# Kernel optimization log

Measured on AMD Instinct MI355X. Metric: run time of the kernel, lower is better.

The kernel has to match this reference:

```python
import jax, jax.numpy as jnp
import numpy as np

B, T, D, H, L = 2, 2048, 2048, 16, 64
HD = D // H  # 128
EPS = 1e-5


def setup_inputs() -> dict:
    key = jax.random.key(0)
    ks = jax.random.split(key, 16)
    s = 0.02
    inp = {
        'x': jax.random.normal(ks[0], (B, T, D), jnp.float32),
        'mask': jnp.tril(jnp.ones((T, T), dtype=bool)),
        'ln_w': jnp.ones((D,), jnp.float32),
        'ln_b': jnp.zeros((D,), jnp.float32),
        'wq': jax.random.normal(ks[1], (D, D), jnp.float32) * s,
        'bq': jnp.zeros((D,), jnp.float32),
        'wk': jax.random.normal(ks[2], (D, D), jnp.float32) * s,
        'bk': jnp.zeros((D,), jnp.float32),
        'wv': jax.random.normal(ks[3], (D, D), jnp.float32) * s,
        'bv': jnp.zeros((D,), jnp.float32),
        'wo': jax.random.normal(ks[4], (D, D), jnp.float32) * s,
        'bo': jnp.zeros((D,), jnp.float32),
        'wcq': jax.random.normal(ks[5], (HD, L), jnp.float32) * s,
        'bcq': jnp.zeros((L,), jnp.float32),
        'wck': jax.random.normal(ks[6], (HD, L), jnp.float32) * s,
        'bck': jnp.zeros((L,), jnp.float32),
        'wcv': jax.random.normal(ks[7], (HD, L), jnp.float32) * s,
        'bcv': jnp.zeros((L,), jnp.float32),
        'wd': jax.random.normal(ks[8], (L, HD), jnp.float32) * s,
        'bd': jnp.zeros((HD,), jnp.float32),
    }
    # standard RoPE frequency table: theta_i = 10000^{-2i/HD}
    inv_freq = 1.0 / (10000.0 ** (jnp.arange(0, HD, 2, dtype=jnp.float32) / HD))
    ang = jnp.arange(T, dtype=jnp.float32)[:, None] * inv_freq[None, :]  # [T, HD/2]
    inp['freqs_cos'] = jnp.cos(ang)
    inp['freqs_sin'] = jnp.sin(ang)
    return inp


def _rope(x, cos, sin):
    # x: [B,T,H,HD]; cos/sin: [T, HD/2]; interleaved (even=real, odd=imag)
    xr, xi = x[..., 0::2], x[..., 1::2]
    c = cos[None, :, None, :]
    sn = sin[None, :, None, :]
    out_r = xr * c - xi * sn
    out_i = xr * sn + xi * c
    return jnp.stack([out_r, out_i], axis=-1).reshape(x.shape)


def reference(x, mask, freqs_cos, freqs_sin, ln_w, ln_b, wq, bq, wk, bk, wv, bv,
              wo, bo, wcq, bcq, wck, bck, wcv, bcv, wd, bd):
    # LayerNorm
    mu = jnp.mean(x, axis=-1, keepdims=True)
    var = jnp.mean(jnp.square(x - mu), axis=-1, keepdims=True)
    xn = (x - mu) / jnp.sqrt(var + EPS) * ln_w + ln_b

    q = (xn @ wq + bq).reshape(B, T, H, HD)
    k = (xn @ wk + bk).reshape(B, T, H, HD)
    v = (xn @ wv + bv).reshape(B, T, H, HD)

    q, k = _rope(q, freqs_cos, freqs_sin), _rope(k, freqs_cos, freqs_sin)

    # compress each head to the latent dim
    q_lat = q @ wcq + bcq  # [B,T,H,L]
    k_lat = k @ wck + bck
    v_lat = v @ wcv + bcv

    scale = 1.0 / np.sqrt(L).astype(np.float32)
    scores = jnp.einsum('bqhl,bkhl->bhqk', q_lat, k_lat) * scale  # [B,H,T,T]
    additive = jnp.where(mask, 0.0, -1e9).astype(scores.dtype)  # bool mask -> additive
    scores = scores + additive[None, None, :, :]
    attn = jax.nn.softmax(scores, axis=-1)

    out = jnp.einsum('bhqk,bkhl->bqhl', attn, v_lat)  # [B,T,H,L]
    out = (out @ wd + bd).reshape(B, T, D)  # decompress to head_dim, merge heads
    return out @ wo + bo
```

## Files before the change

### kernel.cpp

```cpp
#include <hip/hip_runtime.h>
#include <hip/hip_bf16.h>
#include <stdint.h>

#define BB 2
#define TB 2048
#define DB 2048
#define HB 16
#define HDB 128
#define LB 64
#define MB 4096

typedef __hip_bfloat16 bf16;
typedef __attribute__((ext_vector_type(8))) short bf16x8;
typedef __attribute__((ext_vector_type(4))) float f32x4;

#define MFMA_16x16x32 __builtin_amdgcn_mfma_f32_16x16x32_bf16

typedef __attribute__((address_space(3))) void lds_t;
typedef const __attribute__((address_space(1))) void gvm_t;

static __device__ __forceinline__ float bf2f(bf16 h) { return __bfloat162float(h); }
static __device__ __forceinline__ bf16 f2bf(float f) { return __float2bfloat16(f); }
union BV8 { bf16x8 v; bf16 e[8]; };
union BV4 { ushort4 v; bf16 e[4]; };

#define SWZC(r) (((r) ^ ((r) >> 3)) & 7)

__device__ void do_ln(const float* __restrict__ x, const float* __restrict__ g,
                      const float* __restrict__ be, bf16* __restrict__ xn,
                      int row, int tid, char* sm) {
  float* red = (float*)sm;
  const float4* xr = (const float4*)(x + (size_t)row * DB);
  float4 a = xr[2 * tid], b = xr[2 * tid + 1];
  float s = a.x + a.y + a.z + a.w + b.x + b.y + b.z + b.w;
  float s2 = a.x * a.x + a.y * a.y + a.z * a.z + a.w * a.w +
             b.x * b.x + b.y * b.y + b.z * b.z + b.w * b.w;
  for (int off = 32; off > 0; off >>= 1) {
    s += __shfl_down(s, off);
    s2 += __shfl_down(s2, off);
  }
  int w = tid >> 6, lane = tid & 63;
  if (lane == 0) { red[w] = s; red[4 + w] = s2; }
  __syncthreads();
  s = red[0] + red[1] + red[2] + red[3];
  s2 = red[4] + red[5] + red[6] + red[7];
  float mu = s * (1.f / DB);
  float var = s2 * (1.f / DB) - mu * mu;
  float rstd = rsqrtf(var + 1e-5f);
  const float4* gw = (const float4*)g;
  const float4* bb = (const float4*)be;
  float4 g0 = gw[2 * tid], g1 = gw[2 * tid + 1];
  float4 b0 = bb[2 * tid], b1 = bb[2 * tid + 1];
  BV8 u;
  u.e[0] = f2bf((a.x - mu) * rstd * g0.x + b0.x);
  u.e[1] = f2bf((a.y - mu) * rstd * g0.y + b0.y);
  u.e[2] = f2bf((a.z - mu) * rstd * g0.z + b0.z);
  u.e[3] = f2bf((a.w - mu) * rstd * g0.w + b0.w);
  u.e[4] = f2bf((b.x - mu) * rstd * g1.x + b1.x);
  u.e[5] = f2bf((b.y - mu) * rstd * g1.y + b1.y);
  u.e[6] = f2bf((b.z - mu) * rstd * g1.z + b1.z);
  u.e[7] = f2bf((b.w - mu) * rstd * g1.w + b1.w);
  *(bf16x8*)(xn + (size_t)row * DB + tid * 8) = u.v;
}

__device__ void do_wconv(const float* __restrict__ W, bf16* __restrict__ Wt,
                         int bx, int by, int tid, char* sm) {
  float(*t)[33] = (float(*)[33])sm;
  int c0 = bx * 32, r0 = by * 32;
  int tx = tid & 31, ty = tid >> 5;
  for (int p = 0; p < 4; ++p)
    t[ty + 8 * p][tx] = W[(size_t)(r0 + ty + 8 * p) * DB + c0 + tx];
  __syncthreads();
  for (int p = 0; p < 4; ++p)
    Wt[(size_t)(c0 + ty + 8 * p) * DB + r0 + tx] = f2bf(t[tx][ty + 8 * p]);
}

__device__ void do_fold_v(const float* __restrict__ wv, const float* __restrict__ wcv,
                          bf16* __restrict__ BtV, int bx, int h, int tid, char* sm) {
  float(*wvs)[36] = (float(*)[36])sm;
  int k0 = bx * 128;
  int l = tid & 63, ks = tid >> 6;
  float acc[32];
#pragma unroll
  for (int i = 0; i < 32; ++i) acc[i] = 0.f;
  for (int dc = 0; dc < 128; dc += 32) {
    __syncthreads();
    for (int i = tid; i < 128 * 32; i += 256) {
      int kk = i >> 5, dd = i & 31;
      wvs[kk][dd] = wv[(size_t)(k0 + kk) * DB + h * 128 + dc + dd];
    }
    __syncthreads();
    float wr[32];
#pragma unroll
    for (int dd = 0; dd < 32; ++dd) wr[dd] = wcv[(dc + dd) * 64 + l];
#pragma unroll
    for (int i = 0; i < 32; ++i) {
      const float4* row = (const float4*)&wvs[ks * 32 + i][0];
#pragma unroll
      for (int d4 = 0; d4 < 8; ++d4) {
        float4 w4 = row[d4];
        acc[i] += w4.x * wr[d4 * 4] + w4.y * wr[d4 * 4 + 1] +
                  w4.z * wr[d4 * 4 + 2] + w4.w * wr[d4 * 4 + 3];
      }
    }
  }
  bf16* dst = BtV + (size_t)(h * 64 + l) * DB + k0 + ks * 32;
#pragma unroll
  for (int i8 = 0; i8 < 4; ++i8) {
    BV8 u;
#pragma unroll
    for (int j = 0; j < 8; ++j) u.e[j] = f2bf(acc[i8 * 8 + j]);
    *(bf16x8*)(dst + i8 * 8) = u.v;
  }
}

__device__ void do_fold_o(const float* __restrict__ wo, const float* __restrict__ wd,
                          bf16* __restrict__ BtO, int bx, int h, int tid, char* sm) {
  float(*wos)[132] = (float(*)[132])sm;
  int n0 = bx * 128;
  int l = tid & 63, ns = tid >> 6;
  float acc[32];
#pragma unroll
  for (int i = 0; i < 32; ++i) acc[i] = 0.f;
  for (int dc = 0; dc < 128; dc += 32) {
    __syncthreads();
    for (int i = tid; i < 32 * 128; i += 256) {
      int dd = i >> 7, nn = i & 127;
      wos[dd][nn] = wo[(size_t)(h * 128 + dc + dd) * DB + n0 + nn];
    }
    __syncthreads();
    float wr[32];
#pragma unroll
    for (int d4 = 0; d4 < 8; ++d4) {
      float4 w4 = *(const float4*)&wd[l * 128 + dc + d4 * 4];
      wr[d4 * 4] = w4.x; wr[d4 * 4 + 1] = w4.y;
      wr[d4 * 4 + 2] = w4.z; wr[d4 * 4 + 3] = w4.w;
    }
#pragma unroll
    for (int dd = 0; dd < 32; ++dd) {
      float w = wr[dd];
      const float4* row = (const float4*)&wos[dd][ns * 32];
#pragma unroll
      for (int i4 = 0; i4 < 8; ++i4) {
        float4 a4 = row[i4];
        acc[i4 * 4 + 0] += a4.x * w; acc[i4 * 4 + 1] += a4.y * w;
        acc[i4 * 4 + 2] += a4.z * w; acc[i4 * 4 + 3] += a4.w * w;
      }
    }
  }
#pragma unroll
  for (int i = 0; i < 32; ++i)
    BtO[(size_t)(n0 + ns * 32 + i) * 1024 + h * 64 + l] = f2bf(acc[i]);
}

__global__ __launch_bounds__(256) void prep_kernel(
    const float* __restrict__ x, const float* __restrict__ ln_w,
    const float* __restrict__ ln_b, bf16* __restrict__ xn,
    const float* __restrict__ wq, const float* __restrict__ wk,
    bf16* __restrict__ wqkT,
    const float* __restrict__ wv, const float* __restrict__ wcv,
    bf16* __restrict__ BtV,
    const float* __restrict__ wo, const float* __restrict__ wd,
    bf16* __restrict__ BtO,
    const float* __restrict__ bv, const float* __restrict__ bcv,
    float* __restrict__ bvlat,
    const float* __restrict__ bd, const float* __restrict__ bo,
    float* __restrict__ bo2) {
  __shared__ __align__(16) char sm[18432];
  int b = blockIdx.x, tid = threadIdx.x;
  if (b < 4096) {
    do_ln(x, ln_w, ln_b, xn, b, tid, sm);
  } else if (b < 8192) {
    int bb = b - 4096;
    do_wconv(wq, wqkT, bb & 63, bb >> 6, tid, sm);
  } else if (b < 12288) {
    int bb = b - 8192;
    do_wconv(wk, wqkT + (size_t)2048 * 2048, bb & 63, bb >> 6, tid, sm);
  } else if (b < 12544) {
    int bb = b - 12288;
    do_fold_v(wv, wcv, BtV, bb & 15, bb >> 4, tid, sm);
  } else if (b < 12800) {
    int bb = b - 12544;
    do_fold_o(wo, wd, BtO, bb & 15, bb >> 4, tid, sm);
  } else if (b < 12804) {
    int j = (b - 12800) * 256 + tid;
    int h = j >> 6, l = j & 63;
    float s = bcv[l];
    for (int d = 0; d < 128; ++d) s += bv[h * 128 + d] * wcv[d * 64 + l];
    bvlat[j] = s;
  } else {
    float(*red)[64] = (float(*)[64])sm;
    int nl = tid & 63, ks = tid >> 6;
    int n = (b - 12804) * 64 + nl;
    float s = 0.f;
    for (int k = ks * 512; k < ks * 512 + 512; ++k)
      s += bd[k & 127] * wo[(size_t)k * DB + n];
    red[ks][nl] = s;
    __syncthreads();
    if (ks == 0) bo2[n] = bo[n] + red[0][nl] + red[1][nl] + red[2][nl] + red[3][nl];
  }
}

__global__ __launch_bounds__(256) void gemm_qkv_kernel(
    const bf16* __restrict__ A, const bf16* __restrict__ wqkT,
    const bf16* __restrict__ BtV,
    const float* __restrict__ bq, const float* __restrict__ bk,
    const float* __restrict__ bvl,
    const float* __restrict__ wcq, const float* __restrict__ wck,
    const float* __restrict__ bcq, const float* __restrict__ bck,
    bf16* __restrict__ qlat, bf16* __restrict__ klat, bf16* __restrict__ vlatT,
    const float* __restrict__ fcos, const float* __restrict__ fsin) {
  constexpr int K = DB;
  __shared__ __align__(16) char smem[49152];
  bf16* As = (bf16*)smem;
  bf16* Bs = (bf16*)(smem + 8192);
  bf16* Qt = (bf16*)smem;
  bf16* Wt = (bf16*)(smem + 32768);
  int tid = threadIdx.x;
  int m0 = blockIdx.y * 128, n0 = blockIdx.x * 128;
  int w = tid >> 6, l = tid & 63;
  int wr = w >> 1, wc = w & 1;
  int lrow = l & 15, lk = (l >> 4) * 8, ck = l >> 4;
  const bf16* Bsrc = (n0 < 4096) ? (wqkT + (size_t)n0 * K)
                                 : (BtV + (size_t)(n0 - 4096) * K);
  int sel = n0 >> 11;

  if (sel < 2) {
    const float* wcp = sel == 0 ? wcq : wck;
    for (int i = tid; i < 8192; i += 256) {
      int d = i >> 6, jj = i & 63;
      Wt[jj * 128 + (((d >> 3) ^ (jj & 7)) * 8) + (d & 7)] = f2bf(wcp[d * 64 + jj]);
    }
  }

  f32x4 zero4 = {0.f, 0.f, 0.f, 0.f};
  f32x4 acc[4][4];
  for (int m = 0; m < 4; ++m)
    for (int n = 0; n < 4; ++n) acc[m][n] = zero4;

  for (int kk = 0; kk < K / 32; ++kk) {
    int k0 = kk * 32;
    __syncthreads();
#pragma unroll
    for (int i = 0; i < 2; ++i) {
      int c = i * 256 + tid;
      int r = c >> 2, cc = c & 3;
      int cb = i * 256 + (tid & ~63);
      __builtin_amdgcn_global_load_lds(
          (gvm_t*)&A[(size_t)(m0 + r) * K + k0 + cc * 8], (lds_t*)&As[cb * 8], 16, 0, 0);
      __builtin_amdgcn_global_load_lds(
          (gvm_t*)&Bsrc[(size_t)r * K + k0 + cc * 8], (lds_t*)&Bs[cb * 8], 16, 0, 0);
    }
    __syncthreads();
    bf16x8 af[4], bfr[4];
    for (int m = 0; m < 4; ++m)
      af[m] = *(bf16x8*)&As[(wr * 64 + m * 16 + lrow) * 32 + lk];
    for (int n = 0; n < 4; ++n)
      bfr[n] = *(bf16x8*)&Bs[(wc * 64 + n * 16 + lrow) * 32 + lk];
    for (int m = 0; m < 4; ++m)
      for (int n = 0; n < 4; ++n)
        acc[m][n] = MFMA_16x16x32(af[m], bfr[n], acc[m][n], 0, 0, 0);
  }

  int rg = 4 * (l >> 4), cl = l & 15;
  if (sel == 2) {
    for (int mf = 0; mf < 4; ++mf) {
      int rowb = m0 + wr * 64 + mf * 16 + rg;
      for (int nf = 0; nf < 4; ++nf) {
        int col = n0 + wc * 64 + nf * 16 + cl;
        int colV = col - 4096;
        float bv_ = bvl[colV];
        size_t vbase = ((size_t)((rowb >> 11) * HB + (colV >> 6)) * 64 + (colV & 63)) * TB
                       + (rowb & (TB - 1));
        for (int r = 0; r < 4; ++r)
          vlatT[vbase + r] = f2bf(acc[mf][nf][r] + bv_);
      }
    }
    return;
  }

  const float* bias = sel == 0 ? bq : bk;
  __syncthreads();
  for (int mf = 0; mf < 4; ++mf) {
    int rowb = m0 + wr * 64 + mf * 16 + rg;
    int rl0 = wr * 64 + mf * 16 + rg;
    for (int nf = 0; nf < 4; ++nf) {
      int col = n0 + wc * 64 + nf * 16 + cl;
      int colL = col & 2047;
      int cloc = wc * 64 + nf * 16 + cl;
      float bv_ = bias[colL];
      for (int r = 0; r < 4; ++r) {
        int rr = rowb + r;
        float v = acc[mf][nf][r] + bv_;
        float pv = __shfl_xor(v, 1);
        int t = rr & (TB - 1);
        int pi = (col & 127) >> 1;
        float c = fcos[t * 64 + pi], sn = fsin[t * 64 + pi];
        v = (col & 1) ? (pv * sn + v * c) : (v * c - pv * sn);
        int rl = rl0 + r;
        Qt[rl * 128 + ((((cloc >> 3) ^ (rl & 7)) * 8) + (cloc & 7))] = f2bf(v);
      }
    }
  }
  __syncthreads();
  f32x4 pacc[2][4];
#pragma unroll
  for (int mi = 0; mi < 2; ++mi)
#pragma unroll
    for (int nf = 0; nf < 4; ++nf) pacc[mi][nf] = zero4;
#pragma unroll
  for (int kc = 0; kc < 4; ++kc) {
    bf16x8 aq[2], bw[4];
#pragma unroll
    for (int mi = 0; mi < 2; ++mi) {
      int row = w * 32 + mi * 16 + lrow;
      aq[mi] = *(bf16x8*)&Qt[row * 128 + (((kc * 4 + ck) ^ (row & 7)) * 8)];
    }
#pragma unroll
    for (int nf = 0; nf < 4; ++nf) {
      int jrow = nf * 16 + lrow;
      bw[nf] = *(bf16x8*)&Wt[jrow * 128 + (((kc * 4 + ck) ^ (jrow & 7)) * 8)];
    }
#pragma unroll
    for (int mi = 0; mi < 2; ++mi)
#pragma unroll
      for (int nf = 0; nf < 4; ++nf)
        pacc[mi][nf] = MFMA_16x16x32(aq[mi], bw[nf], pacc[mi][nf], 0, 0, 0);
  }
  int head = (n0 & 2047) >> 7;
  const float* bias2 = sel == 0 ? bcq : bck;
  bf16* outp = sel == 0 ? qlat : klat;
#pragma unroll
  for (int mi = 0; mi < 2; ++mi)
#pragma unroll
    for (int nf = 0; nf < 4; ++nf) {
      int colj = nf * 16 + cl;
      float b2 = bias2[colj];
#pragma unroll
      for (int r = 0; r < 4; ++r) {
        int roG = m0 + w * 32 + mi * 16 + rg + r;
        outp[((size_t)roG * HB + head) * 64 + colj] = f2bf(pacc[mi][nf][r] + b2);
      }
    }
}

__global__ __launch_bounds__(256) void gemm_out_kernel(
    const bf16* __restrict__ A, const bf16* __restrict__ Bt,
    const float* __restrict__ bias, float* __restrict__ Cout) {
  constexpr int K = 1024, N = DB;
  __shared__ __align__(16) bf16 As[128 * 32];
  __shared__ __align__(16) bf16 Bs[128 * 32];
  int tid = threadIdx.x;
  int m0 = blockIdx.y * 128, n0 = blockIdx.x * 128;
  int w = tid >> 6, l = tid & 63;
  int wr = w >> 1, wc = w & 1;
  int lrow = l & 15, lk = (l >> 4) * 8;

  f32x4 zero4 = {0.f, 0.f, 0.f, 0.f};
  f32x4 acc[4][4];
  for (int m = 0; m < 4; ++m)
    for (int n = 0; n < 4; ++n) acc[m][n] = zero4;

  for (int kk = 0; kk < K / 32; ++kk) {
    int k0 = kk * 32;
    __syncthreads();
#pragma unroll
    for (int i = 0; i < 2; ++i) {
      int c = i * 256 + tid;
      int r = c >> 2, cc = c & 3;
      int cb = i * 256 + (tid & ~63);
      __builtin_amdgcn_global_load_lds(
          (gvm_t*)&A[(size_t)(m0 + r) * K + k0 + cc * 8], (lds_t*)&As[cb * 8], 16, 0, 0);
      __builtin_amdgcn_global_load_lds(
          (gvm_t*)&Bt[(size_t)(n0 + r) * K + k0 + cc * 8], (lds_t*)&Bs[cb * 8], 16, 0, 0);
    }
    __syncthreads();
    bf16x8 af[4], bfr[4];
    for (int m = 0; m < 4; ++m)
      af[m] = *(bf16x8*)&As[(wr * 64 + m * 16 + lrow) * 32 + lk];
    for (int n = 0; n < 4; ++n)
      bfr[n] = *(bf16x8*)&Bs[(wc * 64 + n * 16 + lrow) * 32 + lk];
    for (int m = 0; m < 4; ++m)
      for (int n = 0; n < 4; ++n)
        acc[m][n] = MFMA_16x16x32(af[m], bfr[n], acc[m][n], 0, 0, 0);
  }

  int rg = 4 * (l >> 4), cl = l & 15;
  for (int m = 0; m < 4; ++m) {
    int rowb = m0 + wr * 64 + m * 16 + rg;
    for (int n = 0; n < 4; ++n) {
      int col = n0 + wc * 64 + n * 16 + cl;
      float bv = bias[col];
      for (int r = 0; r < 4; ++r)
        Cout[(size_t)(rowb + r) * N + col] = acc[m][n][r] + bv;
    }
  }
}

__global__ __launch_bounds__(256) void attn_kernel(const bf16* __restrict__ qlat,
                                                   const bf16* __restrict__ klat,
                                                   const bf16* __restrict__ vlatT,
                                                   bf16* __restrict__ aout) {
  int tid = threadIdx.x, w = tid >> 6, l = tid & 63;
  int job = ((int)blockIdx.x & 7) * 64 + ((int)blockIdx.x >> 3);
  int bh = job >> 4, pair = job & 15;
  int h = bh & 15, b = bh >> 4;
  int lrow = l & 15, ck = l >> 4, hi4 = l >> 4;
  __shared__ __align__(16) bf16 Ks[2][64 * 64];
  __shared__ __align__(16) bf16 VsT[2][64 * 64];
  __shared__ __align__(16) bf16 Ps[4][16 * 64];
  f32x4 zero4 = {0.f, 0.f, 0.f, 0.f};

#define ASTAGE(buf, kv0)                                                          \
  {                                                                               \
    _Pragma("unroll") for (int i = 0; i < 2; ++i) {                               \
      int c = i * 256 + tid;                                                      \
      int row = c >> 3, ch = c & 7;                                               \
      int dst = (c & ~63) * 8;                                                    \
      __builtin_amdgcn_global_load_lds(                                           \
          (gvm_t*)(klat + ((size_t)(b * TB + (kv0) + row) * HB + h) * LB +        \
                   ((ch ^ SWZC(row)) * 8)),                                       \
          (lds_t*)&Ks[buf][dst], 16, 0, 0);                                       \
      __builtin_amdgcn_global_load_lds(                                           \
          (gvm_t*)(vlatT + ((size_t)bh * 64 + row) * TB + (kv0) +                 \
                   ((ch ^ SWZC(row)) * 8)),                                       \
          (lds_t*)&VsT[buf][dst], 16, 0, 0);                                      \
    }                                                                             \
  }

  for (int half = 0; half < 2; ++half) {
    int tile = half ? pair : 31 - pair;
    int q0 = tile * 64;
    const bf16* qp = qlat + ((size_t)(b * TB + q0 + w * 16 + lrow) * HB + h) * LB;
    bf16x8 qf0 = *(const bf16x8*)(qp + ck * 8);
    bf16x8 qf1 = *(const bf16x8*)(qp + 32 + ck * 8);
    float mr = -1e30f, lsum = 0.f;
    f32x4 o[4];
    for (int n = 0; n < 4; ++n) o[n] = zero4;
    int qr = q0 + w * 16 + lrow;
    int swq = SWZC(lrow);

    __syncthreads();
    ASTAGE(0, 0)
    asm volatile("s_waitcnt vmcnt(0)");
    __syncthreads();

    for (int kt = 0; kt <= tile; ++kt) {
      int cur = kt & 1;
      int kv0 = kt * 64;
      if (kt < tile) ASTAGE(cur ^ 1, kv0 + 64)
      f32x4 s[4];
      __builtin_amdgcn_s_setprio(1);
#pragma unroll
      for (int kg = 0; kg < 4; ++kg) {
        int row = kg * 16 + lrow;
        int sw = SWZC(row);
        bf16x8 kf0 = *(bf16x8*)&Ks[cur][row * 64 + ((ck ^ sw) * 8)];
        bf16x8 kf1 = *(bf16x8*)&Ks[cur][row * 64 + (((ck + 4) ^ sw) * 8)];
        f32x4 a = zero4;
        a = MFMA_16x16x32(kf0, qf0, a, 0, 0, 0);
        a = MFMA_16x16x32(kf1, qf1, a, 0, 0, 0);
        s[kg] = a;
      }
      __builtin_amdgcn_s_setprio(0);
      float sc[4][4];
      bool diag = (kt == tile);
#pragma unroll
      for (int kg = 0; kg < 4; ++kg)
#pragma unroll
        for (int r = 0; r < 4; ++r) {
          float v = s[kg][r] * 0.125f;
          if (diag) {
            int kvg = kv0 + kg * 16 + hi4 * 4 + r;
            if (kvg > qr) v = -1e30f;
          }
          sc[kg][r] = v;
        }
      float rm = sc[0][0];
#pragma unroll
      for (int kg = 0; kg < 4; ++kg)
#pragma unroll
        for (int r = 0; r < 4; ++r) rm = fmaxf(rm, sc[kg][r]);
      rm = fmaxf(rm, __shfl_xor(rm, 16));
      rm = fmaxf(rm, __shfl_xor(rm, 32));
      bool resc = __any(rm > mr + 8.f);
      float f = 1.f;
      if (resc) {
        float mn = fmaxf(mr, rm);
        f = __expf(mr - mn);
        mr = mn;
      }
#pragma unroll
      for (int kg = 0; kg < 4; ++kg)
#pragma unroll
        for (int r = 0; r < 4; ++r) sc[kg][r] = __expf(sc[kg][r] - mr);
      float ps = 0.f;
#pragma unroll
      for (int kg = 0; kg < 4; ++kg)
#pragma unroll
        for (int r = 0; r < 4; ++r) ps += sc[kg][r];
      ps += __shfl_xor(ps, 16);
      ps += __shfl_xor(ps, 32);
      lsum = lsum * f + ps;
      if (resc) {
#pragma unroll
        for (int r = 0; r < 4; ++r) {
          float fo = __shfl(f, hi4 * 4 + r, 64);
#pragma unroll
          for (int n = 0; n < 4; ++n) o[n][r] *= fo;
        }
      }
#pragma unroll
      for (int kg = 0; kg < 4; ++kg) {
        BV4 p4;
#pragma unroll
        for (int r = 0; r < 4; ++r) p4.e[r] = f2bf(sc[kg][r]);
        int kvb = kg * 16 + hi4 * 4;
        *(ushort4*)&Ps[w][lrow * 64 + (((kvb >> 3) ^ swq) * 8) + (kvb & 7)] = p4.v;
      }
      bf16x8 pa0 = *(bf16x8*)&Ps[w][lrow * 64 + ((ck ^ swq) * 8)];
      bf16x8 pa1 = *(bf16x8*)&Ps[w][lrow * 64 + (((ck + 4) ^ swq) * 8)];
      __builtin_amdgcn_s_setprio(1);
#pragma unroll
      for (int n = 0; n < 4; ++n) {
        int row = n * 16 + lrow;
        int sw = SWZC(row);
        bf16x8 vf0 = *(bf16x8*)&VsT[cur][row * 64 + ((ck ^ sw) * 8)];
        bf16x8 vf1 = *(bf16x8*)&VsT[cur][row * 64 + (((ck + 4) ^ sw) * 8)];
        o[n] = MFMA_16x16x32(pa0, vf0, o[n], 0, 0, 0);
        o[n] = MFMA_16x16x32(pa1, vf1, o[n], 0, 0, 0);
      }
      __builtin_amdgcn_s_setprio(0);
      asm volatile("s_waitcnt vmcnt(0)");
      __syncthreads();
    }
    float inv[4];
#pragma unroll
    for (int r = 0; r < 4; ++r) {
      float lo = __shfl(lsum, hi4 * 4 + r, 64);
      inv[r] = 1.f / lo;
    }
#pragma unroll
    for (int n = 0; n < 4; ++n)
#pragma unroll
      for (int r = 0; r < 4; ++r) {
        size_t row = (size_t)b * TB + q0 + w * 16 + 4 * hi4 + r;
        aout[(row * HB + h) * LB + n * 16 + lrow] = f2bf(o[n][r] * inv[r]);
      }
  }
#undef ASTAGE
}

extern "C" void kernel_launch(void* const* d_in, const int* in_sizes, int n_in,
                              void* d_out, int out_size, void* d_ws, size_t ws_size,
                              hipStream_t stream) {
  const float* x    = (const float*)d_in[0];
  const float* ln_w = (const float*)d_in[2];
  const float* ln_b = (const float*)d_in[3];
  const float* wq   = (const float*)d_in[4];
  const float* bq   = (const float*)d_in[5];
  const float* wk   = (const float*)d_in[6];
  const float* bk   = (const float*)d_in[7];
  const float* wv   = (const float*)d_in[8];
  const float* bv   = (const float*)d_in[9];
  const float* wo   = (const float*)d_in[10];
  const float* bo   = (const float*)d_in[11];
  const float* wcq  = (const float*)d_in[12];
  const float* bcq  = (const float*)d_in[13];
  const float* wck  = (const float*)d_in[14];
  const float* bck  = (const float*)d_in[15];
  const float* wcv  = (const float*)d_in[16];
  const float* bcv  = (const float*)d_in[17];
  const float* wd   = (const float*)d_in[18];
  const float* bd   = (const float*)d_in[19];
  const float* fcos = (const float*)d_in[20];
  const float* fsin = (const float*)d_in[21];

  char* ws = (char*)d_ws;
  bf16*  xn    = (bf16*)(ws);
  bf16*  wqkT  = (bf16*)(ws + 16777216);
  bf16*  BtV   = (bf16*)(ws + 33554432);
  bf16*  BtO   = (bf16*)(ws + 37748736);
  bf16*  qlat  = (bf16*)(ws + 41943040);
  bf16*  klat  = (bf16*)(ws + 58720256);
  bf16*  vlatT = (bf16*)(ws + 75497472);
  float* bvlat = (float*)(ws + 83886080);
  float* bo2   = (float*)(ws + 83890176);
  bf16*  aoutp = wqkT;

  prep_kernel<<<12836, 256, 0, stream>>>(
      x, ln_w, ln_b, xn, wq, wk, wqkT, wv, wcv, BtV, wo, wd, BtO,
      bv, bcv, bvlat, bd, bo, bo2);

  gemm_qkv_kernel<<<dim3(40, 32), 256, 0, stream>>>(
      xn, wqkT, BtV, bq, bk, bvlat, wcq, wck, bcq, bck,
      qlat, klat, vlatT, fcos, fsin);

  attn_kernel<<<512, 256, 0, stream>>>(qlat, klat, vlatT, aoutp);

  gemm_out_kernel<<<dim3(16, 32), 256, 0, stream>>>(aoutp, BtO, bo2, (float*)d_out);
}
```

Baseline: 283.4 us.

## Process both causal query tiles in one KV pass and vectorize vlatT stores

The attention kernel now runs the two paired query tiles (31-pair and pair) together in a single sweep over KV tiles instead of two separate sweeps. Each K/V tile loaded into LDS is reused by both tiles' MFMAs for as long as the shorter tile is active, which cuts global-to-LDS traffic and barrier count by up to roughly half. In exchange, each thread holds two sets of accumulators and softmax state, raising register pressure. Separately, the V-latent epilogue packs four bf16 values into a single ushort4 store instead of four scalar stores.

After: 295.8 us. +4.4%, slower.

```diff
diff --git a/kernel.cpp b/kernel.cpp
--- a/kernel.cpp
+++ b/kernel.cpp
@@ -272,8 +272,9 @@
         float bv_ = bvl[colV];
         size_t vbase = ((size_t)((rowb >> 11) * HB + (colV >> 6)) * 64 + (colV & 63)) * TB
                        + (rowb & (TB - 1));
-        for (int r = 0; r < 4; ++r)
-          vlatT[vbase + r] = f2bf(acc[mf][nf][r] + bv_);
+        BV4 p4;
+        for (int r = 0; r < 4; ++r) p4.e[r] = f2bf(acc[mf][nf][r] + bv_);
+        *(ushort4*)&vlatT[vbase] = p4.v;
       }
     }
     return;
@@ -428,116 +429,120 @@
     }                                                                             \
   }
 
+#define PROCESS(sX, mrX, lsX, oX, qrX, isDiag)                                    \
+  {                                                                               \
+    float sc[4][4];                                                               \
+    _Pragma("unroll") for (int kg = 0; kg < 4; ++kg)                              \
+      _Pragma("unroll") for (int r = 0; r < 4; ++r) {                             \
+        float v = sX[kg][r] * 0.125f;                                             \
+        if (isDiag) {                                                             \
+          int kvg = kv0 + kg * 16 + hi4 * 4 + r;                                  \
+          if (kvg > qrX) v = -1e30f;                                              \
+        }                                                                         \
+        sc[kg][r] = v;                                                            \
+      }                                                                           \
+    float rm = sc[0][0];                                                          \
+    _Pragma("unroll") for (int kg = 0; kg < 4; ++kg)                              \
+      _Pragma("unroll") for (int r = 0; r < 4; ++r) rm = fmaxf(rm, sc[kg][r]);    \
+    rm = fmaxf(rm, __shfl_xor(rm, 16));                                           \
+    rm = fmaxf(rm, __shfl_xor(rm, 32));                                           \
+    bool resc = __any(rm > mrX + 8.f);                                            \
+    float f = 1.f;                                                                \
+    if (resc) { float mn = fmaxf(mrX, rm); f = __expf(mrX - mn); mrX = mn; }      \
+    _Pragma("unroll") for (int kg = 0; kg < 4; ++kg)                              \
+      _Pragma("unroll") for (int r = 0; r < 4; ++r)                               \
+        sc[kg][r] = __expf(sc[kg][r] - mrX);                                      \
+    float ps = 0.f;                                                               \
+    _Pragma("unroll") for (int kg = 0; kg < 4; ++kg)                              \
+      _Pragma("unroll") for (int r = 0; r < 4; ++r) ps += sc[kg][r];              \
+    ps += __shfl_xor(ps, 16);                                                     \
+    ps += __shfl_xor(ps, 32);                                                     \
+    lsX = lsX * f + ps;                                                           \
+    if (resc) {                                                                   \
+      _Pragma("unroll") for (int r = 0; r < 4; ++r) {                             \
+        float fo = __shfl(f, hi4 * 4 + r, 64);                                    \
+        _Pragma("unroll") for (int n = 0; n < 4; ++n) oX[n][r] *= fo;             \
+      }                                                                           \
+    }                                                                             \
+    _Pragma("unroll") for (int kg = 0; kg < 4; ++kg) {                            \
+      BV4 p4;                                                                     \
+      _Pragma("unroll") for (int r = 0; r < 4; ++r) p4.e[r] = f2bf(sc[kg][r]);    \
+      int kvb = kg * 16 + hi4 * 4;                                                \
+      *(ushort4*)&Ps[w][lrow * 64 + (((kvb >> 3) ^ swq) * 8) + (kvb & 7)] = p4.v; \
+    }                                                                             \
+    bf16x8 pa0 = *(bf16x8*)&Ps[w][lrow * 64 + ((ck ^ swq) * 8)];                  \
+    bf16x8 pa1 = *(bf16x8*)&Ps[w][lrow * 64 + (((ck + 4) ^ swq) * 8)];            \
+    __builtin_amdgcn_s_setprio(1);                                                \
+    _Pragma("unroll") for (int n = 0; n < 4; ++n) {                               \
+      int row = n * 16 + lrow;                                                    \
+      int sw = SWZC(row);                                                         \
+      bf16x8 vf0 = *(bf16x8*)&VsT[cur][row * 64 + ((ck ^ sw) * 8)];               \
+      bf16x8 vf1 = *(bf16x8*)&VsT[cur][row * 64 + (((ck + 4) ^ sw) * 8)];         \
+      oX[n] = MFMA_16x16x32(pa0, vf0, oX[n], 0, 0, 0);                            \
+      oX[n] = MFMA_16x16x32(pa1, vf1, oX[n], 0, 0, 0);                            \
+    }                                                                             \
+    __builtin_amdgcn_s_setprio(0);                                                \
+  }
+
+  int tileA = 31 - pair, tileB = pair;
+  int q0A = tileA * 64, q0B = tileB * 64;
+  int swq = SWZC(lrow);
+  const bf16* qpA = qlat + ((size_t)(b * TB + q0A + w * 16 + lrow) * HB + h) * LB;
+  const bf16* qpB = qlat + ((size_t)(b * TB + q0B + w * 16 + lrow) * HB + h) * LB;
+  bf16x8 qfA0 = *(const bf16x8*)(qpA + ck * 8);
+  bf16x8 qfA1 = *(const bf16x8*)(qpA + 32 + ck * 8);
+  bf16x8 qfB0 = *(const bf16x8*)(qpB + ck * 8);
+  bf16x8 qfB1 = *(const bf16x8*)(qpB + 32 + ck * 8);
+  float mrA = -1e30f, lsA = 0.f, mrB = -1e30f, lsB = 0.f;
+  f32x4 oA[4], oB[4];
+  for (int n = 0; n < 4; ++n) { oA[n] = zero4; oB[n] = zero4; }
+  int qrA = q0A + w * 16 + lrow, qrB = q0B + w * 16 + lrow;
+  int nkt = tileA + 1;
+
+  ASTAGE(0, 0)
+  asm volatile("s_waitcnt vmcnt(0)");
+  __syncthreads();
+
+  for (int kt = 0; kt < nkt; ++kt) {
+    int cur = kt & 1;
+    int kv0 = kt * 64;
+    if (kt + 1 < nkt) ASTAGE(cur ^ 1, kv0 + 64)
+    bool actB = (kt <= tileB);
+    f32x4 sA[4], sB[4];
+    __builtin_amdgcn_s_setprio(1);
+#pragma unroll
+    for (int kg = 0; kg < 4; ++kg) {
+      int row = kg * 16 + lrow;
+      int sw = SWZC(row);
+      bf16x8 kf0 = *(bf16x8*)&Ks[cur][row * 64 + ((ck ^ sw) * 8)];
+      bf16x8 kf1 = *(bf16x8*)&Ks[cur][row * 64 + (((ck + 4) ^ sw) * 8)];
+      f32x4 a = zero4;
+      a = MFMA_16x16x32(kf0, qfA0, a, 0, 0, 0);
+      a = MFMA_16x16x32(kf1, qfA1, a, 0, 0, 0);
+      sA[kg] = a;
+      if (actB) {
+        f32x4 bb = zero4;
+        bb = MFMA_16x16x32(kf0, qfB0, bb, 0, 0, 0);
+        bb = MFMA_16x16x32(kf1, qfB1, bb, 0, 0, 0);
+        sB[kg] = bb;
+      }
+    }
+    __builtin_amdgcn_s_setprio(0);
+    PROCESS(sA, mrA, lsA, oA, qrA, (kt == tileA))
+    if (actB) PROCESS(sB, mrB, lsB, oB, qrB, (kt == tileB))
+    asm volatile("s_waitcnt vmcnt(0)");
+    __syncthreads();
+  }
+
+#pragma unroll
   for (int half = 0; half < 2; ++half) {
-    int tile = half ? pair : 31 - pair;
-    int q0 = tile * 64;
-    const bf16* qp = qlat + ((size_t)(b * TB + q0 + w * 16 + lrow) * HB + h) * LB;
-    bf16x8 qf0 = *(const bf16x8*)(qp + ck * 8);
-    bf16x8 qf1 = *(const bf16x8*)(qp + 32 + ck * 8);
-    float mr = -1e30f, lsum = 0.f;
-    f32x4 o[4];
-    for (int n = 0; n < 4; ++n) o[n] = zero4;
-    int qr = q0 + w * 16 + lrow;
-    int swq = SWZC(lrow);
-
-    __syncthreads();
-    ASTAGE(0, 0)
-    asm volatile("s_waitcnt vmcnt(0)");
-    __syncthreads();
-
-    for (int kt = 0; kt <= tile; ++kt) {
-      int cur = kt & 1;
-      int kv0 = kt * 64;
-      if (kt < tile) ASTAGE(cur ^ 1, kv0 + 64)
-      f32x4 s[4];
-      __builtin_amdgcn_s_setprio(1);
-#pragma unroll
-      for (int kg = 0; kg < 4; ++kg) {
-        int row = kg * 16 + lrow;
-        int sw = SWZC(row);
-        bf16x8 kf0 = *(bf16x8*)&Ks[cur][row * 64 + ((ck ^ sw) * 8)];
-        bf16x8 kf1 = *(bf16x8*)&Ks[cur][row * 64 + (((ck + 4) ^ sw) * 8)];
-        f32x4 a = zero4;
-        a = MFMA_16x16x32(kf0, qf0, a, 0, 0, 0);
-        a = MFMA_16x16x32(kf1, qf1, a, 0, 0, 0);
-        s[kg] = a;
-      }
-      __builtin_amdgcn_s_setprio(0);
-      float sc[4][4];
-      bool diag = (kt == tile);
-#pragma unroll
-      for (int kg = 0; kg < 4; ++kg)
-#pragma unroll
-        for (int r = 0; r < 4; ++r) {
-          float v = s[kg][r] * 0.125f;
-          if (diag) {
-            int kvg = kv0 + kg * 16 + hi4 * 4 + r;
-            if (kvg > qr) v = -1e30f;
-          }
-          sc[kg][r] = v;
-        }
-      float rm = sc[0][0];
-#pragma unroll
-      for (int kg = 0; kg < 4; ++kg)
-#pragma unroll
-        for (int r = 0; r < 4; ++r) rm = fmaxf(rm, sc[kg][r]);
-      rm = fmaxf(rm, __shfl_xor(rm, 16));
-      rm = fmaxf(rm, __shfl_xor(rm, 32));
-      bool resc = __any(rm > mr + 8.f);
-      float f = 1.f;
-      if (resc) {
-        float mn = fmaxf(mr, rm);
-        f = __expf(mr - mn);
-        mr = mn;
-      }
-#pragma unroll
-      for (int kg = 0; kg < 4; ++kg)
-#pragma unroll
-        for (int r = 0; r < 4; ++r) sc[kg][r] = __expf(sc[kg][r] - mr);
-      float ps = 0.f;
-#pragma unroll
-      for (int kg = 0; kg < 4; ++kg)
-#pragma unroll
-        for (int r = 0; r < 4; ++r) ps += sc[kg][r];
-      ps += __shfl_xor(ps, 16);
-      ps += __shfl_xor(ps, 32);
-      lsum = lsum * f + ps;
-      if (resc) {
-#pragma unroll
-        for (int r = 0; r < 4; ++r) {
-          float fo = __shfl(f, hi4 * 4 + r, 64);
-#pragma unroll
-          for (int n = 0; n < 4; ++n) o[n][r] *= fo;
-        }
-      }
-#pragma unroll
-      for (int kg = 0; kg < 4; ++kg) {
-        BV4 p4;
-#pragma unroll
-        for (int r = 0; r < 4; ++r) p4.e[r] = f2bf(sc[kg][r]);
-        int kvb = kg * 16 + hi4 * 4;
-        *(ushort4*)&Ps[w][lrow * 64 + (((kvb >> 3) ^ swq) * 8) + (kvb & 7)] = p4.v;
-      }
-      bf16x8 pa0 = *(bf16x8*)&Ps[w][lrow * 64 + ((ck ^ swq) * 8)];
-      bf16x8 pa1 = *(bf16x8*)&Ps[w][lrow * 64 + (((ck + 4) ^ swq) * 8)];
-      __builtin_amdgcn_s_setprio(1);
-#pragma unroll
-      for (int n = 0; n < 4; ++n) {
-        int row = n * 16 + lrow;
-        int sw = SWZC(row);
-        bf16x8 vf0 = *(bf16x8*)&VsT[cur][row * 64 + ((ck ^ sw) * 8)];
-        bf16x8 vf1 = *(bf16x8*)&VsT[cur][row * 64 + (((ck + 4) ^ sw) * 8)];
-        o[n] = MFMA_16x16x32(pa0, vf0, o[n], 0, 0, 0);
-        o[n] = MFMA_16x16x32(pa1, vf1, o[n], 0, 0, 0);
-      }
-      __builtin_amdgcn_s_setprio(0);
-      asm volatile("s_waitcnt vmcnt(0)");
-      __syncthreads();
-    }
+    float ls = half ? lsB : lsA;
+    int q0 = half ? q0B : q0A;
+    f32x4* o = half ? oB : oA;
     float inv[4];
 #pragma unroll
     for (int r = 0; r < 4; ++r) {
-      float lo = __shfl(lsum, hi4 * 4 + r, 64);
+      float lo = __shfl(ls, hi4 * 4 + r, 64);
       inv[r] = 1.f / lo;
     }
 #pragma unroll
@@ -549,6 +554,7 @@
       }
   }
 #undef ASTAGE
+#undef PROCESS
 }
 
 extern "C" void kernel_launch(void* const* d_in, const int* in_sizes, int n_in,
```
